# Kernel tuning notes

Hardware: AMD Instinct MI355X
Metric: run time of the kernel (lower is better)

## Reference

```python
import jax, jax.numpy as jnp
import numpy as np

N_NODES = 100000
N_EDGES = 1600000
IN_C, HID_C, OUT_C = 26, 128, 64
BN_EPS = 1e-5
WEIGHT_TABLE = jnp.array([0.7,0.9,0.7,0.9,0.3,0.7,0.3,0.9,0.3,0.3,0.9,0.7,0.1,
                          0.9,0.5,0.9,0.5,0.5,0.1,0.3,0.7,0.9,0.9,0.9,0.9,0.9],
                         dtype=jnp.float32)


def setup_inputs() -> dict:
    key = jax.random.key(0)
    ks = jax.random.split(key, 20)
    d = {}
    d['h'] = jax.random.normal(ks[0], (N_NODES, IN_C), dtype=jnp.float32)
    d['src'] = jax.random.randint(ks[1], (N_EDGES,), 0, N_NODES, dtype=jnp.int32)
    d['dst'] = jax.random.randint(ks[2], (N_EDGES,), 0, N_NODES, dtype=jnp.int32)
    # GraphConv weights (Glorot-ish scale)
    d['w0'] = jax.random.normal(ks[3], (IN_C, HID_C), dtype=jnp.float32) * (1.0 / np.sqrt(IN_C))
    d['b0'] = jnp.zeros((HID_C,), jnp.float32)
    d['w1'] = jax.random.normal(ks[4], (HID_C, HID_C), dtype=jnp.float32) * (1.0 / np.sqrt(HID_C))
    d['b1'] = jnp.zeros((HID_C,), jnp.float32)
    d['w2'] = jax.random.normal(ks[5], (HID_C, HID_C), dtype=jnp.float32) * (1.0 / np.sqrt(HID_C))
    d['b2'] = jnp.zeros((HID_C,), jnp.float32)
    # BatchNorm affine params
    for i in range(3):
        d[f'g{i}'] = jnp.ones((HID_C,), jnp.float32)
        d[f'bt{i}'] = jnp.zeros((HID_C,), jnp.float32)
    d['wfc'] = jax.random.normal(ks[6], (HID_C, OUT_C), dtype=jnp.float32) * (1.0 / np.sqrt(HID_C))
    d['bfc'] = jnp.zeros((OUT_C,), jnp.float32)
    return d


def _degree_norms(src, dst):
    ones = jnp.ones((N_EDGES,), jnp.float32)
    deg_out = jax.ops.segment_sum(ones, src, num_segments=N_NODES)
    deg_in = jax.ops.segment_sum(ones, dst, num_segments=N_NODES)
    norm_src = jnp.clip(deg_out, 1.0, None) ** -0.5  # [N]
    norm_dst = jnp.clip(deg_in, 1.0, None) ** -0.5   # [N]
    return norm_src[:, None], norm_dst[:, None]


def _graph_conv(h, W, b, src, dst, norm_src, norm_dst):
    # DGL GraphConv, norm='both': D_dst^{-1/2} A^T D_src^{-1/2} X W + b
    y = (h * norm_src) @ W                                   # [N, out]
    agg = jax.ops.segment_sum(y[src], dst, num_segments=N_NODES)
    return agg * norm_dst + b


def _batch_norm(x, gamma, beta):
    mu = jnp.mean(x, axis=0)
    var = jnp.mean((x - mu) ** 2, axis=0)
    return (x - mu) * jax.lax.rsqrt(var + BN_EPS) * gamma + beta


def reference(h, src, dst, w0, b0, w1, b1, w2, b2,
              g0, bt0, g1, bt1, g2, bt2, wfc, bfc):
    node_cats = jnp.argmax(h, axis=1)
    node_weights = WEIGHT_TABLE[node_cats][:, None]  # [N,1]
    norm_src, norm_dst = _degree_norms(src, dst)
    x = h
    for W, b, g, bt in ((w0, b0, g0, bt0), (w1, b1, g1, bt1), (w2, b2, g2, bt2)):
        x = _graph_conv(x, W, b, src, dst, norm_src, norm_dst)
        x = _batch_norm(x, g, bt)
        x = jax.nn.relu(x)
    out = x @ wfc + bfc
    return out, node_weights
```

## Files before the change

kernel.cpp:

```cpp
#include <hip/hip_runtime.h>

#define NN 100000
#define NE 1600000
#define BN_EPS 1e-5f
#define CSHIFT 9
#define NBC ((NN + 511) >> CSHIFT)
#define CAPC 10240
#define EPB1 4096
#define NBLK1 ((NE + EPB1 - 1)/EPB1)
#define NTILES ((NN + 63)/64)
#define GGRID 521
#define NPAGE 64

typedef short bf16x8 __attribute__((ext_vector_type(8)));
typedef float f32x4  __attribute__((ext_vector_type(4)));

__constant__ float c_wtab[26] = {0.7f,0.9f,0.7f,0.9f,0.3f,0.7f,0.3f,0.9f,0.3f,0.3f,0.9f,0.7f,0.1f,
                                 0.9f,0.5f,0.9f,0.5f,0.5f,0.1f,0.3f,0.7f,0.9f,0.9f,0.9f,0.9f,0.9f};

__device__ __forceinline__ unsigned f2bf(float f){
    unsigned u = __float_as_uint(f);
    return (u + 0x7fffu + ((u >> 16) & 1u)) >> 16;
}
__device__ __forceinline__ float bflo(unsigned v){ return __uint_as_float(v << 16); }
__device__ __forceinline__ float bfhi(unsigned v){ return __uint_as_float(v & 0xffff0000u); }

__global__ void k_prepw(const float* __restrict__ w0, const float* __restrict__ w1,
                        const float* __restrict__ w2, const float* __restrict__ wfc,
                        unsigned short* __restrict__ wt){
    int i = blockIdx.x*256 + threadIdx.x;
    if (i < 4096){
        int c = i >> 5, k = i & 31;
        float v = (k < 26) ? w0[k*128 + c] : 0.f;
        wt[i] = (unsigned short)f2bf(v);
    } else if (i < 20480){
        int j = i - 4096; int c = j >> 7, k = j & 127;
        wt[i] = (unsigned short)f2bf(w1[k*128 + c]);
    } else if (i < 36864){
        int j = i - 20480; int c = j >> 7, k = j & 127;
        wt[i] = (unsigned short)f2bf(w2[k*128 + c]);
    } else if (i < 45056){
        int j = i - 36864; int c = j >> 7, k = j & 127;
        wt[i] = (unsigned short)f2bf(wfc[k*64 + c]);
    }
}

__global__ void k_init(unsigned* __restrict__ gcurD, unsigned* __restrict__ gcurS){
    int i = blockIdx.x*256 + threadIdx.x;
    if (i < NBC){ gcurD[i] = (unsigned)i*CAPC; gcurS[i] = (unsigned)i*CAPC; }
}

__global__ __launch_bounds__(512) void k_radix1(const int* __restrict__ src,
                                                const int* __restrict__ dst,
                                                unsigned* __restrict__ gcurD,
                                                unsigned* __restrict__ gcurS,
                                                unsigned* __restrict__ pairs,
                                                unsigned short* __restrict__ tok){
    __shared__ unsigned hD[NBC], hS[NBC];
    int tid = threadIdx.x;
    for (int i = tid; i < NBC; i += 512){ hD[i] = 0u; hS[i] = 0u; }
    __syncthreads();
    int base = blockIdx.x*EPB1;
    int n = NE - base; if (n > EPB1) n = EPB1;
    for (int k = tid; k < n; k += 512){
        atomicAdd(&hD[(unsigned)dst[base+k] >> CSHIFT], 1u);
        atomicAdd(&hS[(unsigned)src[base+k] >> CSHIFT], 1u);
    }
    __syncthreads();
    for (int i = tid; i < NBC; i += 512){
        unsigned c = hD[i];
        hD[i] = c ? atomicAdd(&gcurD[i], c) : 0u;
        c = hS[i];
        hS[i] = c ? atomicAdd(&gcurS[i], c) : 0u;
    }
    __syncthreads();
    for (int k = tid; k < n; k += 512){
        int d = dst[base+k], s = src[base+k];
        unsigned bb = (unsigned)d >> CSHIFT;
        unsigned p = atomicAdd(&hD[bb], 1u);
        if (p < (bb+1)*CAPC)
            pairs[p] = ((unsigned)(d & 511) << 17) | (unsigned)s;
        bb = (unsigned)s >> CSHIFT;
        p = atomicAdd(&hS[bb], 1u);
        if (p < (bb+1)*CAPC)
            tok[p] = (unsigned short)(s & 511);
    }
}

__global__ __launch_bounds__(1024) void k_radix2(const unsigned* __restrict__ gcurD,
                                                 const unsigned* __restrict__ gcurS,
                                                 const unsigned* __restrict__ pairs,
                                                 const unsigned short* __restrict__ tok,
                                                 int* __restrict__ csr,
                                                 unsigned* __restrict__ offs,
                                                 unsigned* __restrict__ degi,
                                                 unsigned* __restrict__ dego){
    __shared__ unsigned cnt[512], cur[512], scnt[512];
    int b = blockIdx.x, tid = threadIdx.x;
    if (tid < 512){ cnt[tid] = 0u; scnt[tid] = 0u; }
    __syncthreads();
    unsigned baseC = (unsigned)b*CAPC;
    unsigned nD = gcurD[b] - baseC; if (nD > CAPC) nD = CAPC;
    unsigned nS = gcurS[b] - baseC; if (nS > CAPC) nS = CAPC;
    for (unsigned i = tid; i < nD; i += 1024)
        atomicAdd(&cnt[pairs[baseC + i] >> 17], 1u);
    for (unsigned i = tid; i < nS; i += 1024)
        atomicAdd(&scnt[tok[baseC + i]], 1u);
    __syncthreads();
    if (tid < 512) cur[tid] = cnt[tid];
    __syncthreads();
    for (int o = 1; o < 512; o <<= 1){
        unsigned x = 0;
        if (tid < 512 && tid >= o) x = cur[tid - o];
        __syncthreads();
        if (tid < 512) cur[tid] += x;
        __syncthreads();
    }
    if (tid < 512){
        unsigned ex = cur[tid] - cnt[tid];
        int node = (b << CSHIFT) + tid;
        if (node < NN){
            offs[node] = baseC + ex;
            degi[node] = cnt[tid];
            dego[node] = scnt[tid];
        }
        cur[tid] = ex;
    }
    __syncthreads();
    for (unsigned i = tid; i < nD; i += 1024){
        unsigned pr = pairs[baseC + i];
        unsigned p = atomicAdd(&cur[pr >> 17], 1u);
        csr[baseC + p] = (int)(pr & 0x1FFFFu);
    }
}

__global__ void k_node(const float* __restrict__ h, const unsigned* __restrict__ dego,
                       const unsigned* __restrict__ degi, float* __restrict__ nsrc,
                       float* __restrict__ ndst, float* __restrict__ outw,
                       float* __restrict__ xn0){
    int i = blockIdx.x*blockDim.x + threadIdx.x;
    if (i < NN){
        float d0 = (float)dego[i]; d0 = d0 < 1.f ? 1.f : d0;
        float d1 = (float)degi[i]; d1 = d1 < 1.f ? 1.f : d1;
        float ns = rsqrtf(d0);
        nsrc[i] = ns;
        ndst[i] = rsqrtf(d1);
        float row[26];
        #pragma unroll
        for (int c = 0; c < 26; ++c) row[c] = h[(size_t)i*26 + c];
        float best = row[0]; int bi = 0;
        #pragma unroll
        for (int c = 1; c < 26; ++c){ if (row[c] > best){ best = row[c]; bi = c; } }
        outw[i] = c_wtab[bi];
        #pragma unroll
        for (int c = 0; c < 26; ++c) xn0[(size_t)i*32 + c] = row[c]*ns;
        #pragma unroll
        for (int c = 26; c < 32; ++c) xn0[(size_t)i*32 + c] = 0.f;
    }
}

__global__ __launch_bounds__(64) void k_agg0(const float* __restrict__ xn,
                                             const unsigned* __restrict__ offs,
                                             const unsigned* __restrict__ degi,
                                             const int* __restrict__ csr,
                                             unsigned short* __restrict__ agg){
    int node = blockIdx.x*2 + (threadIdx.x >> 5);
    int c = threadIdx.x & 31;
    unsigned beg = offs[node], end = beg + degi[node];
    float acc = 0.f;
    unsigned e = beg;
    for (; e + 4 <= end; e += 4){
        int s0 = csr[e+0], s1 = csr[e+1], s2 = csr[e+2], s3 = csr[e+3];
        float a0 = xn[(size_t)s0*32 + c];
        float a1 = xn[(size_t)s1*32 + c];
        float a2 = xn[(size_t)s2*32 + c];
        float a3 = xn[(size_t)s3*32 + c];
        acc += (a0 + a1) + (a2 + a3);
    }
    for (; e < end; ++e)
        acc += xn[(size_t)csr[e]*32 + c];
    agg[(size_t)node*32 + c] = (unsigned short)f2bf(acc);
}

__global__ __launch_bounds__(64) void k_agg_bf(const uint4* __restrict__ xn,
                                               const unsigned* __restrict__ offs,
                                               const unsigned* __restrict__ degi,
                                               const int* __restrict__ csr,
                                               uint4* __restrict__ agg){
    int node = blockIdx.x;
    int lane = threadIdx.x;
    int g = lane >> 4, q = lane & 15;
    unsigned beg = offs[node], end = beg + degi[node];
    float a[8];
    #pragma unroll
    for (int j = 0; j < 8; ++j) a[j] = 0.f;
    unsigned e = beg + (unsigned)g;
    for (; e + 12 < end; e += 16){
        int s0 = csr[e], s1 = csr[e+4], s2 = csr[e+8], s3 = csr[e+12];
        uint4 v0 = xn[(size_t)s0*16 + q];
        uint4 v1 = xn[(size_t)s1*16 + q];
        uint4 v2 = xn[(size_t)s2*16 + q];
        uint4 v3 = xn[(size_t)s3*16 + q];
        a[0] += bflo(v0.x) + bflo(v1.x) + bflo(v2.x) + bflo(v3.x);
        a[1] += bfhi(v0.x) + bfhi(v1.x) + bfhi(v2.x) + bfhi(v3.x);
        a[2] += bflo(v0.y) + bflo(v1.y) + bflo(v2.y) + bflo(v3.y);
        a[3] += bfhi(v0.y) + bfhi(v1.y) + bfhi(v2.y) + bfhi(v3.y);
        a[4] += bflo(v0.z) + bflo(v1.z) + bflo(v2.z) + bflo(v3.z);
        a[5] += bfhi(v0.z) + bfhi(v1.z) + bfhi(v2.z) + bfhi(v3.z);
        a[6] += bflo(v0.w) + bflo(v1.w) + bflo(v2.w) + bflo(v3.w);
        a[7] += bfhi(v0.w) + bfhi(v1.w) + bfhi(v2.w) + bfhi(v3.w);
    }
    for (; e < end; e += 4){
        uint4 v = xn[(size_t)csr[e]*16 + q];
        a[0] += bflo(v.x); a[1] += bfhi(v.x);
        a[2] += bflo(v.y); a[3] += bfhi(v.y);
        a[4] += bflo(v.z); a[5] += bfhi(v.z);
        a[6] += bflo(v.w); a[7] += bfhi(v.w);
    }
    #pragma unroll
    for (int j = 0; j < 8; ++j){
        a[j] += __shfl_xor(a[j], 16);
        a[j] += __shfl_xor(a[j], 32);
    }
    if (g == 0){
        uint4 o;
        o.x = f2bf(a[0]) | (f2bf(a[1]) << 16);
        o.y = f2bf(a[2]) | (f2bf(a[3]) << 16);
        o.z = f2bf(a[4]) | (f2bf(a[5]) << 16);
        o.w = f2bf(a[6]) | (f2bf(a[7]) << 16);
        agg[(size_t)node*16 + q] = o;
    }
}

template<int CIN, int COUT, bool STATS, bool NDST, bool F32OUT>
__global__ __launch_bounds__(256) void k_gemm_mfma(const unsigned short* __restrict__ A,
                                                   const unsigned short* __restrict__ Bt,
                                                   const float* __restrict__ bias,
                                                   const float* __restrict__ ndst,
                                                   void* __restrict__ Zv,
                                                   float* __restrict__ part){
    constexpr int KD4 = CIN/8;
    constexpr int NT = COUT/16;
    __shared__ char sA[64*CIN*2];
    __shared__ char sB[COUT*CIN*2];
    __shared__ float sS[2][COUT];
    float* Zf = (float*)Zv;
    unsigned short* Zh = (unsigned short*)Zv;
    const int tid = threadIdx.x;
    const int w = tid >> 6, lane = tid & 63;
    const int lrow = lane & 15, kg = lane >> 4;

    const uint4* B4 = (const uint4*)Bt;
    for (int i = tid; i < COUT*KD4; i += 256){
        int cc = i/KD4, c4 = i - cc*KD4;
        *(uint4*)(sB + ((cc*CIN*2 + c4*16) ^ ((cc&7)<<4))) = B4[i];
    }
    if (STATS){
        for (int i = tid; i < 2*COUT; i += 256) (&sS[0][0])[i] = 0.f;
    }

    float cs[NT], cq[NT];
    #pragma unroll
    for (int n = 0; n < NT; ++n){ cs[n] = 0.f; cq[n] = 0.f; }

    const uint4* A4 = (const uint4*)A;
    const uint4 z4 = make_uint4(0,0,0,0);
    for (int t = blockIdx.x; t < NTILES; t += GGRID){
        const int row0 = t*64;
        for (int i = tid; i < 64*KD4; i += 256){
            int r = i/KD4, c4 = i - r*KD4;
            int gr = row0 + r;
            uint4 v = (gr < NN) ? A4[(size_t)gr*KD4 + c4] : z4;
            *(uint4*)(sA + ((r*CIN*2 + c4*16) ^ ((r&7)<<4))) = v;
        }
        __syncthreads();
        f32x4 acc[NT];
        #pragma unroll
        for (int n = 0; n < NT; ++n) acc[n] = (f32x4){0.f,0.f,0.f,0.f};
        const int arow = w*16 + lrow;
        #pragma unroll
        for (int kk = 0; kk < CIN/32; ++kk){
            const int kb = kk*64 + kg*16;
            bf16x8 af = *(const bf16x8*)(sA + ((arow*CIN*2 + kb) ^ ((arow&7)<<4)));
            #pragma unroll
            for (int n = 0; n < NT; ++n){
                int bc = n*16 + lrow;
                bf16x8 bv = *(const bf16x8*)(sB + ((bc*CIN*2 + kb) ^ ((bc&7)<<4)));
                acc[n] = __builtin_amdgcn_mfma_f32_16x16x32_bf16(af, bv, acc[n], 0, 0, 0);
            }
        }
        int grow[4]; float nm[4]; bool val[4];
        #pragma unroll
        for (int j = 0; j < 4; ++j){
            grow[j] = row0 + w*16 + kg*4 + j;
            val[j]  = grow[j] < NN;
            nm[j]   = (NDST && val[j]) ? ndst[grow[j]] : 1.f;
        }
        #pragma unroll
        for (int n = 0; n < NT; ++n){
            int gcol = n*16 + lrow;
            float bv = bias[gcol];
            #pragma unroll
            for (int j = 0; j < 4; ++j){
                float z = acc[n][j]*nm[j] + bv;
                if (val[j]){
                    if (F32OUT) Zf[(size_t)grow[j]*COUT + gcol] = z;
                    else        Zh[(size_t)grow[j]*COUT + gcol] = (unsigned short)f2bf(z);
                    if (STATS){ cs[n] += z; cq[n] += z*z; }
                }
            }
        }
        __syncthreads();
    }
    if (STATS){
        #pragma unroll
        for (int n = 0; n < NT; ++n){
            float s = cs[n], q = cq[n];
            s += __shfl_xor(s, 16); s += __shfl_xor(s, 32);
            q += __shfl_xor(q, 16); q += __shfl_xor(q, 32);
            if (kg == 0){
                atomicAdd(&sS[0][n*16 + lrow], s);
                atomicAdd(&sS[1][n*16 + lrow], q);
            }
        }
        __syncthreads();
        float* pg = part + (size_t)(blockIdx.x & (NPAGE-1))*2*COUT;
        for (int i = tid; i < 2*COUT; i += 256)
            atomicAdd(&pg[i], (&sS[0][0])[i]);
    }
}

__global__ void k_bnfin(const float* __restrict__ part, float* __restrict__ stats,
                        const float* __restrict__ g, const float* __restrict__ bt){
    int c = threadIdx.x;
    float s = 0.f, q = 0.f;
    #pragma unroll 8
    for (int p = 0; p < NPAGE; ++p){
        s += part[p*256 + c];
        q += part[p*256 + 128 + c];
    }
    float mu  = s / (float)NN;
    float var = q / (float)NN - mu*mu;
    if (var < 0.f) var = 0.f;
    float sc = g[c] * rsqrtf(var + BN_EPS);
    stats[256 + c] = sc;
    stats[384 + c] = bt[c] - mu*sc;
}

__global__ void k_bnapply_bf(const unsigned* __restrict__ Xb, const float* __restrict__ stats,
                             const float* __restrict__ nsrc, unsigned* __restrict__ out){
    int idx = blockIdx.x*blockDim.x + threadIdx.x;
    if (idx < NN*64){
        int d = idx & 63;
        int node = idx >> 6;
        int c0 = d << 1;
        unsigned v = Xb[idx];
        float v0 = bflo(v)*stats[256 + c0]     + stats[384 + c0];
        float v1 = bfhi(v)*stats[256 + c0 + 1] + stats[384 + c0 + 1];
        float ns = nsrc ? nsrc[node] : 1.f;
        v0 = v0 > 0.f ? v0*ns : 0.f;
        v1 = v1 > 0.f ? v1*ns : 0.f;
        out[idx] = f2bf(v0) | (f2bf(v1) << 16);
    }
}

extern "C" void kernel_launch(void* const* d_in, const int* in_sizes, int n_in,
                              void* d_out, int out_size, void* d_ws, size_t ws_size,
                              hipStream_t stream) {
    const float* h   = (const float*)d_in[0];
    const int*   src = (const int*)d_in[1];
    const int*   dst = (const int*)d_in[2];
    const float* w0  = (const float*)d_in[3];
    const float* b0  = (const float*)d_in[4];
    const float* w1  = (const float*)d_in[5];
    const float* b1  = (const float*)d_in[6];
    const float* w2  = (const float*)d_in[7];
    const float* b2  = (const float*)d_in[8];
    const float* g0  = (const float*)d_in[9];
    const float* bt0 = (const float*)d_in[10];
    const float* g1  = (const float*)d_in[11];
    const float* bt1 = (const float*)d_in[12];
    const float* g2  = (const float*)d_in[13];
    const float* bt2 = (const float*)d_in[14];
    const float* wfc = (const float*)d_in[15];
    const float* bfc = (const float*)d_in[16];

    float* out   = (float*)d_out;
    float* out_w = out + (size_t)NN*64;

    char* ws = (char*)d_ws;
    size_t off = 0;
    auto alloc = [&](size_t b){ size_t p = off; off += (b + 255) & ~(size_t)255; return ws + p; };

    unsigned*       dego    = (unsigned*)alloc((size_t)NN*4);
    unsigned*       degi    = (unsigned*)alloc((size_t)NN*4);
    float*          nsrc    = (float*)   alloc((size_t)NN*4);
    float*          ndst    = (float*)   alloc((size_t)NN*4);
    unsigned*       offsets = (unsigned*)alloc((size_t)NN*4);
    unsigned*       gcurD   = (unsigned*)alloc((size_t)NBC*4);
    unsigned*       gcurS   = (unsigned*)alloc((size_t)NBC*4);
    float*          stats   = (float*)   alloc(3*512*4);
    float*          spart   = (float*)   alloc(3*(size_t)NPAGE*256*4);
    unsigned short* wt      = (unsigned short*)alloc(45056*2);
    int*            csr     = (int*)     alloc((size_t)NBC*CAPC*4);
    float*          xn0     = (float*)   alloc((size_t)NN*32*4);
    unsigned short* bufA    = (unsigned short*)alloc((size_t)NN*128*2);
    float*          bufB    = (float*)   alloc((size_t)NN*128*4);
    unsigned*       bufC    = (unsigned*)alloc((size_t)NN*64*4);
    (void)ws_size; (void)in_sizes; (void)n_in; (void)out_size;

    unsigned*       pairs = (unsigned*)bufB;
    unsigned short* tok   = (unsigned short*)((char*)bufB + (size_t)NBC*CAPC*4);
    unsigned short* aggB  = (unsigned short*)bufB;

    hipMemsetAsync(spart, 0, 3*(size_t)NPAGE*256*4, stream);

    k_prepw<<<176, 256, 0, stream>>>(w0, w1, w2, wfc, wt);
    k_init<<<1, 256, 0, stream>>>(gcurD, gcurS);
    k_radix1<<<NBLK1, 512, 0, stream>>>(src, dst, gcurD, gcurS, pairs, tok);
    k_radix2<<<NBC, 1024, 0, stream>>>(gcurD, gcurS, pairs, tok, csr, offsets, degi, dego);
    k_node<<<(NN + 255)/256, 256, 0, stream>>>(h, dego, degi, nsrc, ndst, out_w, xn0);

    k_agg0<<<NN/2, 64, 0, stream>>>(xn0, offsets, degi, csr, aggB);
    k_gemm_mfma<32,128,true,true,false><<<GGRID, 256, 0, stream>>>(aggB, wt, b0, ndst, bufA, spart + 0*NPAGE*256);
    k_bnfin<<<1, 128, 0, stream>>>(spart + 0*NPAGE*256, stats + 0*512, g0, bt0);
    k_bnapply_bf<<<(NN*64 + 255)/256, 256, 0, stream>>>((unsigned*)bufA, stats + 0*512, nsrc, bufC);

    k_agg_bf<<<NN, 64, 0, stream>>>((const uint4*)bufC, offsets, degi, csr, (uint4*)aggB);
    k_gemm_mfma<128,128,true,true,false><<<GGRID, 256, 0, stream>>>(aggB, wt + 4096, b1, ndst, bufA, spart + 1*NPAGE*256);
    k_bnfin<<<1, 128, 0, stream>>>(spart + 1*NPAGE*256, stats + 1*512, g1, bt1);
    k_bnapply_bf<<<(NN*64 + 255)/256, 256, 0, stream>>>((unsigned*)bufA, stats + 1*512, nsrc, bufC);

    k_agg_bf<<<NN, 64, 0, stream>>>((const uint4*)bufC, offsets, degi, csr, (uint4*)aggB);
    k_gemm_mfma<128,128,true,true,false><<<GGRID, 256, 0, stream>>>(aggB, wt + 20480, b2, ndst, bufA, spart + 2*NPAGE*256);
    k_bnfin<<<1, 128, 0, stream>>>(spart + 2*NPAGE*256, stats + 2*512, g2, bt2);
    k_bnapply_bf<<<(NN*64 + 255)/256, 256, 0, stream>>>((unsigned*)bufA, stats + 2*512, nullptr, bufC);

    k_gemm_mfma<128,64,false,false,true><<<GGRID, 256, 0, stream>>>((unsigned short*)bufC, wt + 36864, bfc,
                                                                    nullptr, out, nullptr);
}
```

Before: 374.4 us.

## Fuse neighbor aggregation into MFMA GEMM and pack layer-0 features as bf16

Layers 1 and 2 now gather neighbour features inside the GEMM kernel. Each wave aggregates 16 rows straight into swizzled shared memory and then runs the MFMA tile, so the aggregated bf16 matrix is never written to or re-read from global memory. Layer-0 input features are stored as packed bf16 (64 bytes per node instead of 128), and the first aggregation now uses 16-lane edge groups over 4 uint4 chunks. The fused kernel runs on only 521 blocks, so latency hiding for the irregular gathers drops sharply compared with one block per node. The bf16 input also reduces layer-0 precision.

```diff
diff --git a/kernel.cpp b/kernel.cpp
--- a/kernel.cpp
+++ b/kernel.cpp
@@ -137,7 +137,7 @@
 __global__ void k_node(const float* __restrict__ h, const unsigned* __restrict__ dego,
                        const unsigned* __restrict__ degi, float* __restrict__ nsrc,
                        float* __restrict__ ndst, float* __restrict__ outw,
-                       float* __restrict__ xn0){
+                       unsigned* __restrict__ xn0){
     int i = blockIdx.x*blockDim.x + threadIdx.x;
     if (i < NN){
         float d0 = (float)dego[i]; d0 = d0 < 1.f ? 1.f : d0;
@@ -153,65 +153,27 @@
         for (int c = 1; c < 26; ++c){ if (row[c] > best){ best = row[c]; bi = c; } }
         outw[i] = c_wtab[bi];
         #pragma unroll
-        for (int c = 0; c < 26; ++c) xn0[(size_t)i*32 + c] = row[c]*ns;
-        #pragma unroll
-        for (int c = 26; c < 32; ++c) xn0[(size_t)i*32 + c] = 0.f;
-    }
-}
-
-__global__ __launch_bounds__(64) void k_agg0(const float* __restrict__ xn,
+        for (int d = 0; d < 13; ++d)
+            xn0[(size_t)i*16 + d] = f2bf(row[2*d]*ns) | (f2bf(row[2*d+1]*ns) << 16);
+        #pragma unroll
+        for (int d = 13; d < 16; ++d) xn0[(size_t)i*16 + d] = 0u;
+    }
+}
+
+__global__ __launch_bounds__(64) void k_agg0(const uint4* __restrict__ xn,
                                              const unsigned* __restrict__ offs,
                                              const unsigned* __restrict__ degi,
                                              const int* __restrict__ csr,
-                                             unsigned short* __restrict__ agg){
-    int node = blockIdx.x*2 + (threadIdx.x >> 5);
-    int c = threadIdx.x & 31;
-    unsigned beg = offs[node], end = beg + degi[node];
-    float acc = 0.f;
-    unsigned e = beg;
-    for (; e + 4 <= end; e += 4){
-        int s0 = csr[e+0], s1 = csr[e+1], s2 = csr[e+2], s3 = csr[e+3];
-        float a0 = xn[(size_t)s0*32 + c];
-        float a1 = xn[(size_t)s1*32 + c];
-        float a2 = xn[(size_t)s2*32 + c];
-        float a3 = xn[(size_t)s3*32 + c];
-        acc += (a0 + a1) + (a2 + a3);
-    }
-    for (; e < end; ++e)
-        acc += xn[(size_t)csr[e]*32 + c];
-    agg[(size_t)node*32 + c] = (unsigned short)f2bf(acc);
-}
-
-__global__ __launch_bounds__(64) void k_agg_bf(const uint4* __restrict__ xn,
-                                               const unsigned* __restrict__ offs,
-                                               const unsigned* __restrict__ degi,
-                                               const int* __restrict__ csr,
-                                               uint4* __restrict__ agg){
+                                             uint4* __restrict__ agg){
     int node = blockIdx.x;
     int lane = threadIdx.x;
-    int g = lane >> 4, q = lane & 15;
+    int g = lane >> 2, q = lane & 3;
     unsigned beg = offs[node], end = beg + degi[node];
     float a[8];
     #pragma unroll
     for (int j = 0; j < 8; ++j) a[j] = 0.f;
-    unsigned e = beg + (unsigned)g;
-    for (; e + 12 < end; e += 16){
-        int s0 = csr[e], s1 = csr[e+4], s2 = csr[e+8], s3 = csr[e+12];
-        uint4 v0 = xn[(size_t)s0*16 + q];
-        uint4 v1 = xn[(size_t)s1*16 + q];
-        uint4 v2 = xn[(size_t)s2*16 + q];
-        uint4 v3 = xn[(size_t)s3*16 + q];
-        a[0] += bflo(v0.x) + bflo(v1.x) + bflo(v2.x) + bflo(v3.x);
-        a[1] += bfhi(v0.x) + bfhi(v1.x) + bfhi(v2.x) + bfhi(v3.x);
-        a[2] += bflo(v0.y) + bflo(v1.y) + bflo(v2.y) + bflo(v3.y);
-        a[3] += bfhi(v0.y) + bfhi(v1.y) + bfhi(v2.y) + bfhi(v3.y);
-        a[4] += bflo(v0.z) + bflo(v1.z) + bflo(v2.z) + bflo(v3.z);
-        a[5] += bfhi(v0.z) + bfhi(v1.z) + bfhi(v2.z) + bfhi(v3.z);
-        a[6] += bflo(v0.w) + bflo(v1.w) + bflo(v2.w) + bflo(v3.w);
-        a[7] += bfhi(v0.w) + bfhi(v1.w) + bfhi(v2.w) + bfhi(v3.w);
-    }
-    for (; e < end; e += 4){
-        uint4 v = xn[(size_t)csr[e]*16 + q];
+    for (unsigned e = beg + (unsigned)g; e < end; e += 16){
+        uint4 v = xn[(size_t)csr[e]*4 + q];
         a[0] += bflo(v.x); a[1] += bfhi(v.x);
         a[2] += bflo(v.y); a[3] += bfhi(v.y);
         a[4] += bflo(v.z); a[5] += bfhi(v.z);
@@ -219,6 +181,8 @@
     }
     #pragma unroll
     for (int j = 0; j < 8; ++j){
+        a[j] += __shfl_xor(a[j], 4);
+        a[j] += __shfl_xor(a[j], 8);
         a[j] += __shfl_xor(a[j], 16);
         a[j] += __shfl_xor(a[j], 32);
     }
@@ -228,8 +192,136 @@
         o.y = f2bf(a[2]) | (f2bf(a[3]) << 16);
         o.z = f2bf(a[4]) | (f2bf(a[5]) << 16);
         o.w = f2bf(a[6]) | (f2bf(a[7]) << 16);
-        agg[(size_t)node*16 + q] = o;
-    }
+        agg[(size_t)node*4 + q] = o;
+    }
+}
+
+__global__ __launch_bounds__(256) void k_gemm_agg(const uint4* __restrict__ xn,
+                                                  const unsigned* __restrict__ offs,
+                                                  const unsigned* __restrict__ degi,
+                                                  const int* __restrict__ csr,
+                                                  const unsigned short* __restrict__ Bt,
+                                                  const float* __restrict__ bias,
+                                                  const float* __restrict__ ndst,
+                                                  unsigned short* __restrict__ Zh,
+                                                  float* __restrict__ part){
+    __shared__ char sA[64*256];
+    __shared__ char sB[128*256];
+    __shared__ float sS[2][128];
+    const int tid = threadIdx.x;
+    const int w = tid >> 6, lane = tid & 63;
+    const int lrow = lane & 15, kg = lane >> 4;
+
+    const uint4* B4 = (const uint4*)Bt;
+    for (int i = tid; i < 128*16; i += 256){
+        int cc = i >> 4, c4 = i & 15;
+        *(uint4*)(sB + ((cc*256 + c4*16) ^ ((cc&7)<<4))) = B4[i];
+    }
+    for (int i = tid; i < 256; i += 256) (&sS[0][0])[i] = 0.f;
+    __syncthreads();
+
+    float cs[8], cq[8];
+    #pragma unroll
+    for (int n = 0; n < 8; ++n){ cs[n] = 0.f; cq[n] = 0.f; }
+
+    for (int t = blockIdx.x; t < NTILES; t += GGRID){
+        const int row0 = t*64;
+        for (int i = 0; i < 16; ++i){
+            const int r = w*16 + i;
+            const int node = row0 + r;
+            float a[8];
+            #pragma unroll
+            for (int j = 0; j < 8; ++j) a[j] = 0.f;
+            if (node < NN){
+                unsigned beg = offs[node], end = beg + degi[node];
+                unsigned e = beg + (unsigned)kg;
+                for (; e + 12 < end; e += 16){
+                    int s0 = csr[e], s1 = csr[e+4], s2 = csr[e+8], s3 = csr[e+12];
+                    uint4 v0 = xn[(size_t)s0*16 + lrow];
+                    uint4 v1 = xn[(size_t)s1*16 + lrow];
+                    uint4 v2 = xn[(size_t)s2*16 + lrow];
+                    uint4 v3 = xn[(size_t)s3*16 + lrow];
+                    a[0] += bflo(v0.x) + bflo(v1.x) + bflo(v2.x) + bflo(v3.x);
+                    a[1] += bfhi(v0.x) + bfhi(v1.x) + bfhi(v2.x) + bfhi(v3.x);
+                    a[2] += bflo(v0.y) + bflo(v1.y) + bflo(v2.y) + bflo(v3.y);
+                    a[3] += bfhi(v0.y) + bfhi(v1.y) + bfhi(v2.y) + bfhi(v3.y);
+                    a[4] += bflo(v0.z) + bflo(v1.z) + bflo(v2.z) + bflo(v3.z);
+                    a[5] += bfhi(v0.z) + bfhi(v1.z) + bfhi(v2.z) + bfhi(v3.z);
+                    a[6] += bflo(v0.w) + bflo(v1.w) + bflo(v2.w) + bflo(v3.w);
+                    a[7] += bfhi(v0.w) + bfhi(v1.w) + bfhi(v2.w) + bfhi(v3.w);
+                }
+                for (; e < end; e += 4){
+                    uint4 v = xn[(size_t)csr[e]*16 + lrow];
+                    a[0] += bflo(v.x); a[1] += bfhi(v.x);
+                    a[2] += bflo(v.y); a[3] += bfhi(v.y);
+                    a[4] += bflo(v.z); a[5] += bfhi(v.z);
+                    a[6] += bflo(v.w); a[7] += bfhi(v.w);
+                }
+            }
+            #pragma unroll
+            for (int j = 0; j < 8; ++j){
+                a[j] += __shfl_xor(a[j], 16);
+                a[j] += __shfl_xor(a[j], 32);
+            }
+            if (kg == 0){
+                uint4 o;
+                o.x = f2bf(a[0]) | (f2bf(a[1]) << 16);
+                o.y = f2bf(a[2]) | (f2bf(a[3]) << 16);
+                o.z = f2bf(a[4]) | (f2bf(a[5]) << 16);
+                o.w = f2bf(a[6]) | (f2bf(a[7]) << 16);
+                *(uint4*)(sA + ((r*256 + lrow*16) ^ ((r&7)<<4))) = o;
+            }
+        }
+        f32x4 acc[8];
+        #pragma unroll
+        for (int n = 0; n < 8; ++n) acc[n] = (f32x4){0.f,0.f,0.f,0.f};
+        const int arow = w*16 + lrow;
+        #pragma unroll
+        for (int kk = 0; kk < 4; ++kk){
+            const int kb = kk*64 + kg*16;
+            bf16x8 af = *(const bf16x8*)(sA + ((arow*256 + kb) ^ ((arow&7)<<4)));
+            #pragma unroll
+            for (int n = 0; n < 8; ++n){
+                int bc = n*16 + lrow;
+                bf16x8 bv = *(const bf16x8*)(sB + ((bc*256 + kb) ^ ((bc&7)<<4)));
+                acc[n] = __builtin_amdgcn_mfma_f32_16x16x32_bf16(af, bv, acc[n], 0, 0, 0);
+            }
+        }
+        int grow[4]; float nm[4]; bool val[4];
+        #pragma unroll
+        for (int j = 0; j < 4; ++j){
+            grow[j] = row0 + w*16 + kg*4 + j;
+            val[j]  = grow[j] < NN;
+            nm[j]   = val[j] ? ndst[grow[j]] : 1.f;
+        }
+        #pragma unroll
+        for (int n = 0; n < 8; ++n){
+            int gcol = n*16 + lrow;
+            float bv = bias[gcol];
+            #pragma unroll
+            for (int j = 0; j < 4; ++j){
+                float z = acc[n][j]*nm[j] + bv;
+                if (val[j]){
+                    Zh[(size_t)grow[j]*128 + gcol] = (unsigned short)f2bf(z);
+                    cs[n] += z; cq[n] += z*z;
+                }
+            }
+        }
+    }
+    #pragma unroll
+    for (int n = 0; n < 8; ++n){
+        float s = cs[n], q = cq[n];
+        s += __shfl_xor(s, 16); s += __shfl_xor(s, 32);
+        q += __shfl_xor(q, 16); q += __shfl_xor(q, 32);
+        if (kg == 0){
+            atomicAdd(&sS[0][n*16 + lrow], s);
+            atomicAdd(&sS[1][n*16 + lrow], q);
+        }
+    }
+    __syncthreads();
+    float* pg = part + (size_t)(blockIdx.x & (NPAGE-1))*256;
+    for (int i = tid; i < 256; i += 256)
+        atomicAdd(&pg[i], (&sS[0][0])[i]);
 }
 
 template<int CIN, int COUT, bool STATS, bool NDST, bool F32OUT>
@@ -403,7 +495,7 @@
     float*          spart   = (float*)   alloc(3*(size_t)NPAGE*256*4);
     unsigned short* wt      = (unsigned short*)alloc(45056*2);
     int*            csr     = (int*)     alloc((size_t)NBC*CAPC*4);
-    float*          xn0     = (float*)   alloc((size_t)NN*32*4);
+    unsigned*       xn0     = (unsigned*)alloc((size_t)NN*16*4);
     unsigned short* bufA    = (unsigned short*)alloc((size_t)NN*128*2);
     float*          bufB    = (float*)   alloc((size_t)NN*128*4);
     unsigned*       bufC    = (unsigned*)alloc((size_t)NN*64*4);
@@ -411,7 +503,7 @@
 
     unsigned*       pairs = (unsigned*)bufB;
     unsigned short* tok   = (unsigned short*)((char*)bufB + (size_t)NBC*CAPC*4);
-    unsigned short* aggB  = (unsigned short*)bufB;
+    uint4*          aggB  = (uint4*)bufB;
 
     hipMemsetAsync(spart, 0, 3*(size_t)NPAGE*256*4, stream);
 
@@ -421,18 +513,19 @@
     k_radix2<<<NBC, 1024, 0, stream>>>(gcurD, gcurS, pairs, tok, csr, offsets, degi, dego);
     k_node<<<(NN + 255)/256, 256, 0, stream>>>(h, dego, degi, nsrc, ndst, out_w, xn0);
 
-    k_agg0<<<NN/2, 64, 0, stream>>>(xn0, offsets, degi, csr, aggB);
-    k_gemm_mfma<32,128,true,true,false><<<GGRID, 256, 0, stream>>>(aggB, wt, b0, ndst, bufA, spart + 0*NPAGE*256);
+    k_agg0<<<NN, 64, 0, stream>>>((const uint4*)xn0, offsets, degi, csr, aggB);
+    k_gemm_mfma<32,128,true,true,false><<<GGRID, 256, 0, stream>>>((const unsigned short*)aggB, wt, b0,
+                                                                   ndst, bufA, spart + 0*NPAGE*256);
     k_bnfin<<<1, 128, 0, stream>>>(spart + 0*NPAGE*256, stats + 0*512, g0, bt0);
     k_bnapply_bf<<<(NN*64 + 255)/256, 256, 0, stream>>>((unsigned*)bufA, stats + 0*512, nsrc, bufC);
 
-    k_agg_bf<<<NN, 64, 0, stream>>>((const uint4*)bufC, offsets, degi, csr, (uint4*)aggB);
-    k_gemm_mfma<128,128,true,true,false><<<GGRID, 256, 0, stream>>>(aggB, wt + 4096, b1, ndst, bufA, spart + 1*NPAGE*256);
+    k_gemm_agg<<<GGRID, 256, 0, stream>>>((const uint4*)bufC, offsets, degi, csr,
+                                          wt + 4096, b1, ndst, bufA, spart + 1*NPAGE*256);
     k_bnfin<<<1, 128, 0, stream>>>(spart + 1*NPAGE*256, stats + 1*512, g1, bt1);
     k_bnapply_bf<<<(NN*64 + 255)/256, 256, 0, stream>>>((unsigned*)bufA, stats + 1*512, nsrc, bufC);
 
-    k_agg_bf<<<NN, 64, 0, stream>>>((const uint4*)bufC, offsets, degi, csr, (uint4*)aggB);
-    k_gemm_mfma<128,128,true,true,false><<<GGRID, 256, 0, stream>>>(aggB, wt + 20480, b2, ndst, bufA, spart + 2*NPAGE*256);
+    k_gemm_agg<<<GGRID, 256, 0, stream>>>((const uint4*)bufC, offsets, degi, csr,
+                                          wt + 20480, b2, ndst, bufA, spart + 2*NPAGE*256);
     k_bnfin<<<1, 128, 0, stream>>>(spart + 2*NPAGE*256, stats + 2*512, g2, bt2);
     k_bnapply_bf<<<(NN*64 + 255)/256, 256, 0, stream>>>((unsigned*)bufA, stats + 2*512, nullptr, bufC);
 
```

Result: slower. 896.8 us (+139.5%).
